# Optimization experiments

Hardware: AMD Instinct MI355X
Metric: run time of the kernel (lower is better)

The kernel has to match this reference:

```python
import jax, jax.numpy as jnp
import numpy as np

B, T, C, H, W = 8, 8, 32, 16, 28
NH, DK = 4, 8                 # n_head, d_k == d_v
RADIUS = [3, 3, 3, 3]
DILATION = [1, 3, 5, 7]
LN_EPS = 1e-5


def setup_inputs() -> dict:
    key = jax.random.key(0)
    ks = jax.random.split(key, 8)
    s = 1.0 / np.sqrt(C).astype(np.float32)
    return {
        "first": jax.random.normal(ks[0], (B, T, C, H, W), jnp.float32),
        "x": jax.random.normal(ks[1], (B, T, C, H, W), jnp.float32),
        "Wq": jax.random.normal(ks[2], (NH * DK, C), jnp.float32) * s,
        "Wk": jax.random.normal(ks[3], (NH * DK, C), jnp.float32) * s,
        "Wv": jax.random.normal(ks[4], (NH * DK, C), jnp.float32) * s,
        "Wo": jax.random.normal(ks[5], (C, NH * DK), jnp.float32) * s,
        "ln_gamma": 1.0 + 0.1 * jax.random.normal(ks[6], (DK, H, W), jnp.float32),
        "ln_beta": 0.1 * jax.random.normal(ks[7], (DK, H, W), jnp.float32),
    }


def _shift(x, dy, dx):
    # out[..., i, j] = x[..., i+dy, j+dx]; zero out-of-bounds. mask: (H, W) valid.
    h, w = x.shape[-2:]
    xs = jnp.roll(x, (-dy, -dx), axis=(-2, -1))
    mh = (jnp.arange(h) + dy >= 0) & (jnp.arange(h) + dy < h)
    mw = (jnp.arange(w) + dx >= 0) & (jnp.arange(w) + dx < w)
    m = mh[:, None] & mw[None, :]
    return jnp.where(m, xs, 0.0), m


def _head_attn(q, k, v, radius, dilation, scale):
    # q,k,v: (b,t,c,h,w). Returns softmaxed scores P (b,t,O*t,h,w) and
    # aggregation T (b,t,c,h,w). Aggregation uses RAW scaled scores (as the repo
    # does: spatial_temporal_aggregation receives M_A_i, not its softmax).
    b, t, c, h, w = q.shape
    scores, vals, masks = [], [], []
    for dy in range(-radius, radius + 1):
        for dx in range(-radius, radius + 1):
            ks, m = _shift(k, dy * dilation, dx * dilation)
            vs, _ = _shift(v, dy * dilation, dx * dilation)
            # score against all source frames s at the shifted spatial location
            scores.append(jnp.einsum('btchw,bschw->btshw', q, ks))
            vals.append(vs)
            masks.append(m)
    A = jnp.stack(scores, axis=2)                      # (b,t,O,s,h,w), O=(2r+1)^2
    M = jnp.stack(masks, axis=0)                       # (O,h,w)
    A = jnp.where(M[None, None, :, None], A / scale, -jnp.inf)
    O = A.shape[2]
    P = jax.nn.softmax(A.reshape(b, t, O * t, h, w), axis=2)
    Wm = jnp.where(M[None, None, :, None], A, 0.0)     # skip invalid (-inf) slots
    V = jnp.stack(vals, axis=0)                        # (O,b,s,c,h,w)
    Tout = jnp.einsum('btoshw,obschw->btchw', Wm, V)
    return P, Tout


def reference(first, x, Wq, Wk, Wv, Wo, ln_gamma, ln_beta):
    b, t, c, h, w = x.shape
    q = jnp.einsum('btchw,oc->btohw', first, Wq).reshape(b, t, NH, DK, h, w)
    k = jnp.einsum('btchw,oc->btohw', x, Wk).reshape(b, t, NH, DK, h, w)
    v = jnp.einsum('btchw,oc->btohw', x, Wv).reshape(b, t, NH, DK, h, w)
    scale = float(np.sqrt(C / NH))
    Ps, Ts = [], []
    for i in range(NH):
        qi = q[:, :, i]
        mu = jnp.mean(qi, axis=(2, 3, 4), keepdims=True)
        var = jnp.var(qi, axis=(2, 3, 4), keepdims=True)
        qi = (qi - mu) / jnp.sqrt(var + LN_EPS) * ln_gamma + ln_beta
        P, Ti = _head_attn(qi, k[:, :, i], v[:, :, i], RADIUS[i], DILATION[i], scale)
        Ps.append(P)
        Ts.append(Ti)
    M_S = jnp.max(jnp.concatenate(Ps, axis=2), axis=2)   # (b,t,h,w)
    M_T = jnp.concatenate(Ts, axis=2)                    # (b,t,NH*DK,h,w)
    out = jnp.einsum('btchw,oc->btohw', M_T, Wo) * M_S[:, :, None]
    return out
```

## Files before the change

### kernel.cpp

```cpp
#include <hip/hip_runtime.h>

#define Bc 8
#define Tc 8
#define Cc 32
#define Hc 16
#define Wc 28
#define NHc 4
#define DKc 8
#define HWc (Hc*Wc)
#define INV_SCALE 0.35355339059327373f
#define LOG2E 1.4426950408889634f
#define LN2f 0.6931471805599453f
#define LN_EPSc 1e-5f

#if __has_builtin(__builtin_amdgcn_exp2f)
#define EXP2f(x) __builtin_amdgcn_exp2f(x)
#else
#define EXP2f(x) exp2f(x)
#endif

typedef _Float16 half8  __attribute__((ext_vector_type(8)));
typedef _Float16 half2v __attribute__((ext_vector_type(2)));
typedef float    f2     __attribute__((ext_vector_type(2)));

union H8 { half8 v; half2v h2[4]; };
union F4 { float4 f4; f2 p[2]; };


__global__ __launch_bounds__(448) void qkv_ln_kernel(
    const float* __restrict__ first, const float* __restrict__ x,
    const float* __restrict__ Wq, const float* __restrict__ Wk,
    const float* __restrict__ Wv,
    const float* __restrict__ gamma, const float* __restrict__ beta,
    half8* __restrict__ Qh, half8* __restrict__ Kh, float* __restrict__ V)
{
    int blk  = blockIdx.x;
    int head = blk >> 6;
    int bt   = blk & 63;
    int t    = bt % Tc;
    int b    = bt / Tc;
    int tid  = threadIdx.x;

    const float* fp = first + (size_t)bt * Cc * HWc + tid;
    const float* xp = x     + (size_t)bt * Cc * HWc + tid;
    float fv[Cc], xv[Cc];
#pragma unroll
    for (int c = 0; c < Cc; ++c) { fv[c] = fp[c*HWc]; xv[c] = xp[c*HWc]; }

    float qv[DKc], kv[DKc], vv[DKc];
#pragma unroll
    for (int dk = 0; dk < DKc; ++dk) {
        int o = head*DKc + dk;
        float aq = 0.f, ak = 0.f, av = 0.f;
#pragma unroll
        for (int c = 0; c < Cc; ++c) {
            aq = fmaf(Wq[o*Cc+c], fv[c], aq);
            ak = fmaf(Wk[o*Cc+c], xv[c], ak);
            av = fmaf(Wv[o*Cc+c], xv[c], av);
        }
        qv[dk] = aq; kv[dk] = ak; vv[dk] = av;
    }

    int bh = b*NHc + head;
    half8 kh;
#pragma unroll
    for (int dk = 0; dk < DKc; ++dk) kh[dk] = (_Float16)kv[dk];
    Kh[((size_t)bh*Tc + t)*HWc + tid] = kh;

    float* vp = V + (((size_t)bh*Tc + t)*HWc + tid)*DKc;
    *(float4*)(vp)   = make_float4(vv[0],vv[1],vv[2],vv[3]);
    *(float4*)(vp+4) = make_float4(vv[4],vv[5],vv[6],vv[7]);

    float s1 = 0.f, s2 = 0.f;
#pragma unroll
    for (int dk = 0; dk < DKc; ++dk) { s1 += qv[dk]; s2 += qv[dk]*qv[dk]; }
#pragma unroll
    for (int off = 32; off >= 1; off >>= 1) {
        s1 += __shfl_down(s1, off, 64);
        s2 += __shfl_down(s2, off, 64);
    }
    __shared__ float r1[8], r2[8];
    int wid = tid >> 6, lane = tid & 63;
    if (lane == 0) { r1[wid] = s1; r2[wid] = s2; }
    __syncthreads();
    float S1 = 0.f, S2 = 0.f;
#pragma unroll
    for (int wv2 = 0; wv2 < 7; ++wv2) { S1 += r1[wv2]; S2 += r2[wv2]; }
    const float invN = 1.f / (float)(DKc * HWc);
    float mu   = S1 * invN;
    float var  = S2 * invN - mu*mu;
    float rstd = rsqrtf(var + LN_EPSc);

    const float QSCALE = INV_SCALE * LOG2E;
    half8 qh;
#pragma unroll
    for (int dk = 0; dk < DKc; ++dk) {
        float gg = gamma[dk*HWc + tid];
        float bb = beta [dk*HWc + tid];
        qh[dk] = (_Float16)(((qv[dk] - mu) * rstd * gg + bb) * QSCALE);
    }
    Qh[((size_t)bh*Tc + t)*HWc + tid] = qh;
}

template<int DIL>
__device__ __forceinline__ void attn_body(
    int bh, int s, int t0, int tid,
    const half8* __restrict__ Qh, const half8* __restrict__ Kh,
    const float* __restrict__ V,
    half8* __restrict__ Tpart, float2* __restrict__ LMpart,
    half8* sK, float4* sV0, float4* sV1)
{
    int w = tid % Wc;
    int h = tid / Wc;

    sK[tid] = Kh[((size_t)bh*Tc + s)*HWc + tid];
    const float* vp = V + ((size_t)bh*Tc + s)*HWc*DKc;
    sV0[tid] = *(const float4*)(vp + tid*DKc);
    sV1[tid] = *(const float4*)(vp + tid*DKc + 4);
    if (tid == 0) {
        half8 z = {};
        sK[HWc]  = z;
        sV0[HWc] = make_float4(0.f,0.f,0.f,0.f);
        sV1[HWc] = make_float4(0.f,0.f,0.f,0.f);
    }

    H8 q[4];
#pragma unroll
    for (int j = 0; j < 4; ++j)
        q[j].v = Qh[((size_t)bh*Tc + (t0+j))*HWc + tid];

    int nvy = 0, nvx = 0;
#pragma unroll
    for (int d = -3; d <= 3; ++d) {
        nvy += ((unsigned)(h + d*DIL) < (unsigned)Hc);
        nvx += ((unsigned)(w + d*DIL) < (unsigned)Wc);
    }
    float corr = (float)(nvy * (7 - nvx));

    f2 a[4][4];
    float l[4], m[4];
#pragma unroll
    for (int j = 0; j < 4; ++j) {
#pragma unroll
        for (int u = 0; u < 4; ++u) a[j][u] = (f2){0.f, 0.f};
        l[j] = 0.f; m[j] = -1e30f;
    }

    __syncthreads();

#pragma unroll
    for (int dy = -3; dy <= 3; ++dy) {
        int hy = h + dy*DIL;
        if ((unsigned)hy >= (unsigned)Hc) continue;
        int rowbase = hy*Wc;
#pragma unroll
        for (int dx = -3; dx <= 3; ++dx) {
            int wx = w + dx*DIL;
            bool cv = (unsigned)wx < (unsigned)Wc;
            int idx = cv ? (rowbase + wx) : HWc;
            H8 k; k.v = sK[idx];
            F4 v0, v1; v0.f4 = sV0[idx]; v1.f4 = sV1[idx];
#pragma unroll
            for (int j = 0; j < 4; ++j) {
                float sc = __builtin_amdgcn_fdot2(q[j].h2[0], k.h2[0],
                           __builtin_amdgcn_fdot2(q[j].h2[1], k.h2[1],
                           __builtin_amdgcn_fdot2(q[j].h2[2], k.h2[2],
                           __builtin_amdgcn_fdot2(q[j].h2[3], k.h2[3],
                                                  0.f, false), false), false), false);
                m[j] = fmaxf(m[j], sc);
                l[j] += EXP2f(sc);
                f2 sc2 = {sc, sc};
                a[j][0] = __builtin_elementwise_fma(sc2, v0.p[0], a[j][0]);
                a[j][1] = __builtin_elementwise_fma(sc2, v0.p[1], a[j][1]);
                a[j][2] = __builtin_elementwise_fma(sc2, v1.p[0], a[j][2]);
                a[j][3] = __builtin_elementwise_fma(sc2, v1.p[1], a[j][3]);
            }
        }
    }

    half8*  tp  = Tpart  + (size_t)(bh*Tc + s)*Tc*HWc + tid;
    float2* lmp = LMpart + (size_t)(bh*Tc + s)*Tc*HWc + tid;
#pragma unroll
    for (int j = 0; j < 4; ++j) {
        half8 hv;
#pragma unroll
        for (int u = 0; u < 4; ++u) {
            hv[2*u]   = (_Float16)(a[j][u][0] * LN2f);
            hv[2*u+1] = (_Float16)(a[j][u][1] * LN2f);
        }
        tp [(t0+j)*HWc] = hv;
        lmp[(t0+j)*HWc] = make_float2(l[j] - corr, m[j]);
    }
}

__global__ __launch_bounds__(448, 4) void attn_kernel(
    const half8* __restrict__ Qh, const half8* __restrict__ Kh,
    const float* __restrict__ V,
    half8* __restrict__ Tpart, float2* __restrict__ LMpart)
{
    int blk = blockIdx.x;
    int p   = blk >> 8;
    int i   = blk & 255;
    int b   = i >> 5;
    int ha  = (i >> 4) & 1;
    int s   = (i >> 1) & 7;
    int th  = i & 1;

    int head = p ? (3 - ha) : ha;
    int bh   = b*NHc + head;
    int t0   = th*4;
    int tid  = threadIdx.x;

    __shared__ half8  sK [HWc+1];
    __shared__ float4 sV0[HWc+1], sV1[HWc+1];

    if      (head == 0) attn_body<1>(bh, s, t0, tid, Qh, Kh, V, Tpart, LMpart, sK, sV0, sV1);
    else if (head == 1) attn_body<3>(bh, s, t0, tid, Qh, Kh, V, Tpart, LMpart, sK, sV0, sV1);
    else if (head == 2) attn_body<5>(bh, s, t0, tid, Qh, Kh, V, Tpart, LMpart, sK, sV0, sV1);
    else                attn_body<7>(bh, s, t0, tid, Qh, Kh, V, Tpart, LMpart, sK, sV0, sV1);
}

__global__ __launch_bounds__(448) void outproj_kernel(
    const half8* __restrict__ Tpart, const float2* __restrict__ LMpart,
    const float* __restrict__ Wo, float* __restrict__ out)
{
    int blk = blockIdx.x;
    int og  = blk >> 6;
    int bt  = blk & 63;
    int b   = bt >> 3, t = bt & 7;
    int tid = threadIdx.x;

    float mv[Cc];
    float MS = 0.f;
#pragma unroll
    for (int head = 0; head < NHc; ++head) {
        int bh = b*NHc + head;
        float acc[DKc];
#pragma unroll
        for (int j = 0; j < DKc; ++j) acc[j] = 0.f;
        float lsum = 0.f, mmax = -1e30f;
#pragma unroll
        for (int s = 0; s < Tc; ++s) {
            half8 u = Tpart[(size_t)((bh*Tc + s)*Tc + t)*HWc + tid];
#pragma unroll
            for (int j = 0; j < DKc; ++j) acc[j] += (float)u[j];
            float2 lm = LMpart[(size_t)((bh*Tc + s)*Tc + t)*HWc + tid];
            lsum += lm.x; mmax = fmaxf(mmax, lm.y);
        }
#pragma unroll
        for (int j = 0; j < DKc; ++j) mv[head*DKc + j] = acc[j];
        MS = fmaxf(MS, EXP2f(mmax) / lsum);
    }
#pragma unroll
    for (int i = 0; i < 8; ++i) {
        int o = og*8 + i;
        float a = 0.f;
#pragma unroll
        for (int c = 0; c < Cc; ++c) a = fmaf(Wo[o*Cc+c], mv[c], a);
        out[((size_t)bt*Cc + o)*HWc + tid] = a * MS;
    }
}

extern "C" void kernel_launch(void* const* d_in, const int* in_sizes, int n_in,
                              void* d_out, int out_size, void* d_ws, size_t ws_size,
                              hipStream_t stream) {
    const float* first = (const float*)d_in[0];
    const float* x     = (const float*)d_in[1];
    const float* Wq    = (const float*)d_in[2];
    const float* Wk    = (const float*)d_in[3];
    const float* Wv    = (const float*)d_in[4];
    const float* Wo    = (const float*)d_in[5];
    const float* g     = (const float*)d_in[6];
    const float* bta   = (const float*)d_in[7];
    float* out = (float*)d_out;

    float* ws = (float*)d_ws;
    const size_t N5 = (size_t)Bc*NHc*Tc*HWc*DKc;
    half8*  Qh  = (half8*)ws;
    half8*  Kh  = (half8*)(ws + N5/2);
    float*  V   = ws + N5;
    half8*  Tp  = (half8*)(ws + 2*N5);
    float2* LMp = (float2*)(ws + 6*N5);

    qkv_ln_kernel <<<Bc*Tc*NHc, 448, 0, stream>>>(first, x, Wq, Wk, Wv, g, bta, Qh, Kh, V);
    attn_kernel   <<<512,       448, 0, stream>>>(Qh, Kh, V, Tp, LMp);
    outproj_kernel<<<256,       448, 0, stream>>>(Tp, LMp, Wo, out);
}
```

Measured before the change: 113.0 us.

## Split outproj reduction across heads per thread and share partials via LDS

The output projection kernel now has each block handle a quarter of the spatial positions, with all four heads. Each thread reduces one head's Tpart/LMpart partials instead of all four output groups re-reading every head's partials. Results go through shared memory, and Wo is also staged there. Previously each of four output-group blocks redundantly reduced all partials. Now each partial is read once, at the cost of an LDS round trip and a barrier.

```diff
diff --git a/kernel.cpp b/kernel.cpp
--- a/kernel.cpp
+++ b/kernel.cpp
@@ -220,44 +220,71 @@
     else                attn_body<7>(bh, s, t0, tid, Qh, Kh, V, Tpart, LMpart, sK, sV0, sV1);
 }
 
+#define MVS 41
+
 __global__ __launch_bounds__(448) void outproj_kernel(
     const half8* __restrict__ Tpart, const float2* __restrict__ LMpart,
     const float* __restrict__ Wo, float* __restrict__ out)
 {
     int blk = blockIdx.x;
-    int og  = blk >> 6;
+    int hq  = blk >> 6;
     int bt  = blk & 63;
     int b   = bt >> 3, t = bt & 7;
     int tid = threadIdx.x;
 
-    float mv[Cc];
-    float MS = 0.f;
-#pragma unroll
-    for (int head = 0; head < NHc; ++head) {
-        int bh = b*NHc + head;
+    __shared__ float smv[112*MVS];
+    __shared__ float swo[Cc*Cc];
+
+    for (int i = tid; i < Cc*Cc; i += 448) swo[i] = Wo[i];
+
+    {
+        int head = tid / 112;
+        int u    = tid - head*112;
+        int hw   = hq*112 + u;
+        int bh   = b*NHc + head;
+
         float acc[DKc];
 #pragma unroll
         for (int j = 0; j < DKc; ++j) acc[j] = 0.f;
         float lsum = 0.f, mmax = -1e30f;
 #pragma unroll
         for (int s = 0; s < Tc; ++s) {
-            half8 u = Tpart[(size_t)((bh*Tc + s)*Tc + t)*HWc + tid];
-#pragma unroll
-            for (int j = 0; j < DKc; ++j) acc[j] += (float)u[j];
-            float2 lm = LMpart[(size_t)((bh*Tc + s)*Tc + t)*HWc + tid];
+            half8 uvec = Tpart[(size_t)((bh*Tc + s)*Tc + t)*HWc + hw];
+#pragma unroll
+            for (int j = 0; j < DKc; ++j) acc[j] += (float)uvec[j];
+            float2 lm = LMpart[(size_t)((bh*Tc + s)*Tc + t)*HWc + hw];
             lsum += lm.x; mmax = fmaxf(mmax, lm.y);
         }
-#pragma unroll
-        for (int j = 0; j < DKc; ++j) mv[head*DKc + j] = acc[j];
-        MS = fmaxf(MS, EXP2f(mmax) / lsum);
-    }
-#pragma unroll
-    for (int i = 0; i < 8; ++i) {
-        int o = og*8 + i;
-        float a = 0.f;
-#pragma unroll
-        for (int c = 0; c < Cc; ++c) a = fmaf(Wo[o*Cc+c], mv[c], a);
-        out[((size_t)bt*Cc + o)*HWc + tid] = a * MS;
+        float* row = smv + u*MVS;
+#pragma unroll
+        for (int j = 0; j < DKc; ++j) row[head*DKc + j] = acc[j];
+        row[32 + head] = lsum;
+        row[36 + head] = mmax;
+    }
+    __syncthreads();
+
+    {
+        int oq = tid / 112;
+        int u  = tid - oq*112;
+        const float* row = smv + u*MVS;
+
+        float MS = 0.f;
+#pragma unroll
+        for (int hh = 0; hh < NHc; ++hh)
+            MS = fmaxf(MS, EXP2f(row[36 + hh]) / row[32 + hh]);
+
+        float mv[Cc];
+#pragma unroll
+        for (int c = 0; c < Cc; ++c) mv[c] = row[c];
+
+#pragma unroll
+        for (int i = 0; i < 8; ++i) {
+            int o = oq*8 + i;
+            float a = 0.f;
+#pragma unroll
+            for (int c = 0; c < Cc; ++c) a = fmaf(swo[o*Cc + c], mv[c], a);
+            out[((size_t)bt*Cc + o)*HWc + hq*112 + u] = a * MS;
+        }
     }
 }
 
```

After: 111.1 us. No clear change (-1.7%).
